# Optimization experiments

Measured on AMD Instinct MI355X. Metric: run time of the kernel, lower is better.

The kernel has to match this reference:

```python
import jax, jax.numpy as jnp
import numpy as np

NUM_CLASSES = 80
CONF_THRE = 0.2
NMS_THRE = 0.45
MAX_DET = 300   # fixed cap replacing torch's variable-length NMS output (padded + keep mask)
IMG = 640.0


def setup_inputs() -> dict:
    key = jax.random.key(0)
    k1, k2 = jax.random.split(key)
    pred = jax.random.uniform(k1, (32, 8400, 85), dtype=jnp.float32)
    # scale cx,cy,w,h to pixel range so IoU/NMS geometry is realistic
    pred = pred.at[..., :4].multiply(IMG)
    zone = jax.random.uniform(k2, (8, 2), dtype=jnp.float32) * IMG
    return {"prediction": pred, "zone": zone}


def _pairwise_iou(b):
    # b: [B, K, 4] in x1y1x2y2
    area = jnp.clip(b[..., 2] - b[..., 0], 0.0) * jnp.clip(b[..., 3] - b[..., 1], 0.0)
    lt = jnp.maximum(b[:, :, None, :2], b[:, None, :, :2])
    rb = jnp.minimum(b[:, :, None, 2:], b[:, None, :, 2:])
    wh = jnp.clip(rb - lt, 0.0)
    inter = wh[..., 0] * wh[..., 1]
    return inter / (area[:, :, None] + area[:, None, :] - inter + 1e-9)


def _postprocess(prediction):
    # decode cx,cy,w,h -> x1,y1,x2,y2
    xy = prediction[..., :2]
    wh = prediction[..., 2:4]
    boxes = jnp.concatenate([xy - wh * 0.5, xy + wh * 0.5], axis=-1)  # [B,N,4]
    obj = prediction[..., 4]                                           # [B,N]
    cls = prediction[..., 5:5 + NUM_CLASSES]
    class_conf = jnp.max(cls, axis=-1)                                 # [B,N]
    class_pred = jnp.argmax(cls, axis=-1)                              # [B,N]

    # confidence mask (obj * class_conf >= thre); invalid -> -inf so top_k drops them
    nms_score = obj * class_conf
    nms_score = jnp.where(nms_score >= CONF_THRE, nms_score, -jnp.inf)

    s, idx = jax.lax.top_k(nms_score, MAX_DET)                         # [B,K]
    b = jnp.take_along_axis(boxes, idx[..., None], axis=1)             # [B,K,4]

    # class-agnostic greedy NMS on score-sorted boxes (matches torchvision.ops.nms)
    iou = _pairwise_iou(b)                                             # [B,K,K]
    keep = jnp.isfinite(s)                                             # valid (passed conf) entries
    ar = jnp.arange(MAX_DET)
    def body(i, keep):
        sup = keep[:, i][:, None] & (iou[:, i, :] > NMS_THRE) & (ar > i)
        return keep & jnp.logical_not(sup)
    keep = jax.lax.fori_loop(0, MAX_DET, body, keep)

    obj_s = jnp.take_along_axis(obj, idx, axis=1)
    conf_s = jnp.take_along_axis(class_conf, idx, axis=1)
    cls_s = jnp.take_along_axis(class_pred, idx, axis=1).astype(jnp.int32)
    # extract_boxes_scores_and_classes: score = max over columns [obj, class_conf]
    scores = jnp.maximum(obj_s, conf_s)
    return b, scores, cls_s, keep


def _points_inside_zone(px, py, zone):
    # px, py: [B,K]; zone: [Z,2]. Ray-casting parity test (faithful to torch version).
    zr = jnp.roll(zone, shift=1, axis=0)
    xi, yi = zone[:, 0], zone[:, 1]
    xj, yj = zr[:, 0], zr[:, 1]
    pyb = py[..., None]  # [B,K,1] vs [Z]
    pxb = px[..., None]
    gyi = yi > pyb
    gyj = yj > pyb
    gx = (xj - xi) * (pyb - yi) / (yj - yi) + xi
    inter = (gyi != gyj) & (gx > pxb)
    return (jnp.sum(inter.astype(jnp.int32), axis=-1) % 2) > 0


def reference(prediction, zone):
    b, scores, classes, keep = _postprocess(prediction)
    cx = (b[..., 0] + b[..., 2]) * 0.5
    cy = (b[..., 1] + b[..., 3]) * 0.5
    in_zone = _points_inside_zone(cx, cy, zone) & keep
    centers_yx = jnp.stack([cy, cx], axis=-1)                          # [B,K,2]
    boxes_yxyx = jnp.stack([b[..., 1], b[..., 0], b[..., 3], b[..., 2]], axis=-1)
    return boxes_yxyx, in_zone, scores, classes, centers_yx, keep
```

## Files before the change

### kernel.cpp

```cpp
#include <hip/hip_runtime.h>
#include <stdint.h>

typedef unsigned long long ull;

#define NA 8400
#define NB 32
#define KTOP 300
#define NC 80
#define CH 33

#define O1 38400
#define O2 48000
#define O3 57600
#define O4 67200
#define O5 86400

__global__ __launch_bounds__(256) void score_kernel(const float* __restrict__ pred,
                                                    uint32_t* __restrict__ keys) {
    __shared__ float sP[128 * 85];
    const int blk = blockIdx.x;
    const float4* g4 = (const float4*)(pred + (size_t)blk * 128 * 85);
    float4* l4 = (float4*)sP;
    for (int i = threadIdx.x; i < (128 * 85 / 4); i += 256) l4[i] = g4[i];
    __syncthreads();
    const int t = threadIdx.x;
    if (t < 128) {
        const float* p = sP + t * 85;
        float obj = p[4];
        float b0 = p[5], b1 = p[6], b2 = p[7], b3 = p[8];
        #pragma unroll
        for (int c = 4; c < NC; c += 4) {
            b0 = fmaxf(b0, p[5 + c]);
            b1 = fmaxf(b1, p[6 + c]);
            b2 = fmaxf(b2, p[7 + c]);
            b3 = fmaxf(b3, p[8 + c]);
        }
        float best = fmaxf(fmaxf(b0, b1), fmaxf(b2, b3));
        float sc = obj * best;
        uint32_t u = (sc >= 0.2f) ? (__float_as_uint(sc) | 0x80000000u) : 0x007FFFFFu;
        keys[(size_t)blk * 128 + t] = u;
    }
}

__global__ __launch_bounds__(256) void batch_kernel(const float* __restrict__ pred,
                                                    const float* __restrict__ zone,
                                                    const uint32_t* __restrict__ keys,
                                                    float* __restrict__ out) {
    #pragma clang fp contract(off)
    __shared__ union {
        uint32_t keys[8448];
        struct {
            float b0[KTOP], b1[KTOP], b2[KTOP], b3[KTOP];
            ull mask[KTOP * 5];
        } late;
    } u;
    __shared__ ull sSel[KTOP];
    __shared__ ull sSorted[KTOP];
    __shared__ uint32_t sH[8 * 257];
    __shared__ uint32_t sTot[4];
    __shared__ uint32_t sBc[2];
    __shared__ int sCnt;
    __shared__ ull sKeepF[5];
    __shared__ float sZone[16];

    const int b = blockIdx.x;
    const int t = threadIdx.x;
    const int lane = t & 63;
    const int wv = t >> 6;
    const int hc = t >> 5;

    {
        const uint4* g4 = (const uint4*)(keys + (size_t)b * NA);
        uint4* l4 = (uint4*)u.keys;
        for (int i = t; i < NA / 4; i += 256) l4[i] = g4[i];
        for (int e = NA + t; e < 8448; e += 256) u.keys[e] = 0u;
    }
    if (t < 16) sZone[t] = zone[t];
    if (t == 0) sCnt = 0;
    __syncthreads();

    uint32_t prefix = 0, r = KTOP;
    const int beg = t * CH;
    const int end = (beg + CH < NA) ? beg + CH : NA;
    for (int round = 0; round < 4; ++round) {
        const int shift = 24 - 8 * round;
        for (int i = t; i < 8 * 257; i += 256) sH[i] = 0u;
        __syncthreads();
        const uint32_t pmask = (round == 0) ? 0u : (0xFFFFFFFFu << (shift + 8));
        for (int e = beg; e < end; ++e) {
            uint32_t k = u.keys[e];
            if ((k & pmask) == (prefix & pmask))
                atomicAdd(&sH[hc * 257 + ((k >> shift) & 0xFFu)], 1u);
        }
        __syncthreads();
        uint32_t v = 0;
        #pragma unroll
        for (int c = 0; c < 8; ++c) v += sH[c * 257 + t];
        uint32_t s = v;
        #pragma unroll
        for (int off = 1; off < 64; off <<= 1) {
            uint32_t o = __shfl_down(s, off, 64);
            if (lane + off < 64) s += o;
        }
        if (lane == 0) sTot[wv] = s;
        __syncthreads();
        uint32_t S = s;
        #pragma unroll
        for (int w2 = 0; w2 < 4; ++w2) if (w2 > wv) S += sTot[w2];
        uint32_t above = S - v;
        if (above < r && S >= r) {
            sBc[0] = prefix | ((uint32_t)t << shift);
            sBc[1] = r - above;
        }
        __syncthreads();
        prefix = sBc[0]; r = sBc[1];
    }
    const uint32_t kth = prefix;
    const uint32_t rem = r;
    const uint32_t cntgt = KTOP - rem;

    {
        uint32_t eqc = 0;
        for (int e = beg; e < end; ++e) {
            uint32_t k = u.keys[e];
            if (k > kth) {
                int p = atomicAdd(&sCnt, 1);
                sSel[p] = ((ull)k << 32) | (ull)(0xFFFFFFFFu - (uint32_t)e);
            } else if (k == kth) eqc++;
        }
        uint32_t ps = eqc;
        #pragma unroll
        for (int off = 1; off < 64; off <<= 1) {
            uint32_t o = __shfl_up(ps, off, 64);
            if (lane >= off) ps += o;
        }
        if (lane == 63) sTot[wv] = ps;
        __syncthreads();
        uint32_t off0 = ps - eqc;
        #pragma unroll
        for (int w2 = 0; w2 < 4; ++w2) if (w2 < wv) off0 += sTot[w2];
        for (int e = beg; e < end; ++e) {
            uint32_t k = u.keys[e];
            if (k == kth) {
                if (off0 < rem)
                    sSel[cntgt + off0] = ((ull)k << 32) | (ull)(0xFFFFFFFFu - (uint32_t)e);
                off0++;
            }
        }
        __syncthreads();
    }

    {
        ull my0 = sSel[t];
        ull my1 = (t < KTOP - 256) ? sSel[256 + t] : 0ull;
        int r0 = 0, r1 = 0;
        for (int j = 0; j < KTOP; ++j) {
            ull v = sSel[j];
            r0 += (v > my0) ? 1 : 0;
            r1 += (v > my1) ? 1 : 0;
        }
        sSorted[r0] = my0;
        if (t < KTOP - 256) sSorted[r1] = my1;
        __syncthreads();
    }

    for (int i = t; i < KTOP; i += 256) {
        uint32_t a = 0xFFFFFFFFu - (uint32_t)sSorted[i];
        const float* p = pred + ((size_t)b * NA + a) * 85;
        float x = p[0], y = p[1], w = p[2], h = p[3];
        float hw = w * 0.5f, hh = h * 0.5f;
        u.late.b0[i] = x - hw; u.late.b1[i] = y - hh;
        u.late.b2[i] = x + hw; u.late.b3[i] = y + hh;
    }
    __syncthreads();

    for (int role = 0; role < 5; ++role) {
        const int j0 = role * 64;
        int jmax = j0 + 64; if (jmax > KTOP) jmax = KTOP;
        for (int i = t; i < KTOP; i += 256) {
            float x1 = u.late.b0[i], y1 = u.late.b1[i], x2 = u.late.b2[i], y2 = u.late.b3[i];
            float ai = fmaxf(x2 - x1, 0.0f) * fmaxf(y2 - y1, 0.0f);
            ull bits = 0ull;
            int jbeg = (j0 > i + 1) ? j0 : (i + 1);
            for (int j = jbeg; j < jmax; ++j) {
                float bx1 = u.late.b0[j], by1 = u.late.b1[j], bx2 = u.late.b2[j], by2 = u.late.b3[j];
                float aj = fmaxf(bx2 - bx1, 0.0f) * fmaxf(by2 - by1, 0.0f);
                float iw = fminf(x2, bx2) - fmaxf(x1, bx1); iw = fmaxf(iw, 0.0f);
                float ih = fminf(y2, by2) - fmaxf(y1, by1); ih = fmaxf(ih, 0.0f);
                float inter = iw * ih;
                float den = ai + aj;
                den = den - inter;
                den = den + 1e-9f;
                float iou = inter / den;
                if (iou > 0.45f) bits |= (1ull << (j - j0));
            }
            u.late.mask[i * 5 + role] = bits;
        }
    }
    __syncthreads();

    if (wv == 0) {
        ull rm[5][5];
        ull kw[5];
        #pragma unroll
        for (int w = 0; w < 5; ++w) {
            int i = w * 64 + lane;
            bool f = (i < KTOP) && (((uint32_t)(sSorted[i] >> 32)) > 0x007FFFFFu);
            kw[w] = __ballot(f);
            #pragma unroll
            for (int ww = 0; ww < 5; ++ww)
                rm[w][ww] = (i < KTOP) ? u.late.mask[i * 5 + ww] : 0ull;
        }
        #pragma unroll
        for (int w = 0; w < 5; ++w) {
            ull cur = kw[w];
            while (cur) {
                int ib = __builtin_ctzll(cur);
                ull m0 = __shfl(rm[w][0], ib);
                ull m1 = __shfl(rm[w][1], ib);
                ull m2 = __shfl(rm[w][2], ib);
                ull m3 = __shfl(rm[w][3], ib);
                ull m4 = __shfl(rm[w][4], ib);
                kw[0] &= ~m0; kw[1] &= ~m1; kw[2] &= ~m2; kw[3] &= ~m3; kw[4] &= ~m4;
                ull done = (ib == 63) ? 0ull : (~0ull << (ib + 1));
                cur = kw[w] & done;
            }
        }
        if (lane == 0) {
            #pragma unroll
            for (int w = 0; w < 5; ++w) sKeepF[w] = kw[w];
        }
    } else {
        const size_t bo = (size_t)b * KTOP;
        for (int i = t - 64; i < KTOP; i += 192) {
            uint32_t a = 0xFFFFFFFFu - (uint32_t)sSorted[i];
            const float* p = pred + ((size_t)b * NA + a) * 85;
            float x = p[0], y = p[1], w = p[2], h = p[3], obj = p[4];
            float best = p[5]; int bc = 0;
            for (int c = 1; c < NC; ++c) {
                float v = p[5 + c];
                if (v > best) { best = v; bc = c; }
            }
            float hw = w * 0.5f, hh = h * 0.5f;
            float x1 = x - hw, y1 = y - hh, x2 = x + hw, y2 = y + hh;
            out[(bo + i) * 4 + 0] = y1;
            out[(bo + i) * 4 + 1] = x1;
            out[(bo + i) * 4 + 2] = y2;
            out[(bo + i) * 4 + 3] = x2;
            out[O4 + (bo + i) * 2 + 0] = (y1 + y2) * 0.5f;
            out[O4 + (bo + i) * 2 + 1] = (x1 + x2) * 0.5f;
            out[O2 + bo + i] = fmaxf(obj, best);
            out[O3 + bo + i] = (float)bc;
        }
    }
    __syncthreads();

    const size_t bo = (size_t)b * KTOP;
    for (int i = t; i < KTOP; i += 256) {
        int kp = (int)((sKeepF[i >> 6] >> (i & 63)) & 1ull);
        float cy = (u.late.b1[i] + u.late.b3[i]) * 0.5f;
        float cx = (u.late.b0[i] + u.late.b2[i]) * 0.5f;
        int cnt = 0;
        #pragma unroll
        for (int e = 0; e < 8; ++e) {
            float xi = sZone[2 * e], yi = sZone[2 * e + 1];
            int ep = (e + 7) & 7;
            float xj = sZone[2 * ep], yj = sZone[2 * ep + 1];
            bool gyi = yi > cy, gyj = yj > cy;
            if (gyi != gyj) {
                float gx = (xj - xi) * (cy - yi) / (yj - yi) + xi;
                if (gx > cx) cnt++;
            }
        }
        int inz = (((cnt & 1) != 0) && kp) ? 1 : 0;
        out[O1 + bo + i] = (float)inz;
        out[O5 + bo + i] = (float)kp;
    }
}

extern "C" void kernel_launch(void* const* d_in, const int* in_sizes, int n_in,
                              void* d_out, int out_size, void* d_ws, size_t ws_size,
                              hipStream_t stream) {
    const float* pred = (const float*)d_in[0];
    const float* zone = (const float*)d_in[1];
    float* out = (float*)d_out;
    uint32_t* keys = (uint32_t*)d_ws;

    score_kernel<<<(NB * NA) / 128, 256, 0, stream>>>(pred, keys);
    batch_kernel<<<NB, 256, 0, stream>>>(pred, zone, keys, out);
}
```

Baseline: 226.6 us.

## Widen per-batch kernel to 1024 threads and parallelize selection and IoU stages

The per-image kernel now runs 1024 threads per block instead of 256. That shortens each thread's radix-select scan chunk from 33 to 9 elements and uses 16 histogram copies to spread atomic contention. The IoU mask stage is flattened over (row, role) pairs, and output writing plus class argmax move before the NMS stage so every thread does its share. Since only 32 blocks run, this adds parallelism inside each block to fill a sparsely used GPU, at the cost of more barrier overhead and higher register pressure.

Result: faster. 200.3 us (-11.6%).

```diff
diff --git a/kernel.cpp b/kernel.cpp
--- a/kernel.cpp
+++ b/kernel.cpp
@@ -7,7 +7,9 @@
 #define NB 32
 #define KTOP 300
 #define NC 80
-#define CH 33
+#define CH 9
+#define NCOPY 16
+#define HSTRIDE 257
 
 #define O1 38400
 #define O2 48000
@@ -42,10 +44,10 @@
     }
 }
 
-__global__ __launch_bounds__(256) void batch_kernel(const float* __restrict__ pred,
-                                                    const float* __restrict__ zone,
-                                                    const uint32_t* __restrict__ keys,
-                                                    float* __restrict__ out) {
+__global__ __launch_bounds__(1024) void batch_kernel(const float* __restrict__ pred,
+                                                     const float* __restrict__ zone,
+                                                     const uint32_t* __restrict__ keys,
+                                                     float* __restrict__ out) {
     #pragma clang fp contract(off)
     __shared__ union {
         uint32_t keys[8448];
@@ -56,8 +58,9 @@
     } u;
     __shared__ ull sSel[KTOP];
     __shared__ ull sSorted[KTOP];
-    __shared__ uint32_t sH[8 * 257];
-    __shared__ uint32_t sTot[4];
+    __shared__ uint32_t sH[NCOPY * HSTRIDE];
+    __shared__ uint32_t sWTot[16];
+    __shared__ uint32_t sTot4[4];
     __shared__ uint32_t sBc[2];
     __shared__ int sCnt;
     __shared__ ull sKeepF[5];
@@ -67,13 +70,11 @@
     const int t = threadIdx.x;
     const int lane = t & 63;
     const int wv = t >> 6;
-    const int hc = t >> 5;
 
     {
         const uint4* g4 = (const uint4*)(keys + (size_t)b * NA);
         uint4* l4 = (uint4*)u.keys;
-        for (int i = t; i < NA / 4; i += 256) l4[i] = g4[i];
-        for (int e = NA + t; e < 8448; e += 256) u.keys[e] = 0u;
+        for (int i = t; i < NA / 4; i += 1024) l4[i] = g4[i];
     }
     if (t < 16) sZone[t] = zone[t];
     if (t == 0) sCnt = 0;
@@ -84,33 +85,38 @@
     const int end = (beg + CH < NA) ? beg + CH : NA;
     for (int round = 0; round < 4; ++round) {
         const int shift = 24 - 8 * round;
-        for (int i = t; i < 8 * 257; i += 256) sH[i] = 0u;
+        for (int i = t; i < NCOPY * HSTRIDE; i += 1024) sH[i] = 0u;
         __syncthreads();
         const uint32_t pmask = (round == 0) ? 0u : (0xFFFFFFFFu << (shift + 8));
         for (int e = beg; e < end; ++e) {
             uint32_t k = u.keys[e];
             if ((k & pmask) == (prefix & pmask))
-                atomicAdd(&sH[hc * 257 + ((k >> shift) & 0xFFu)], 1u);
-        }
-        __syncthreads();
-        uint32_t v = 0;
-        #pragma unroll
-        for (int c = 0; c < 8; ++c) v += sH[c * 257 + t];
-        uint32_t s = v;
-        #pragma unroll
-        for (int off = 1; off < 64; off <<= 1) {
-            uint32_t o = __shfl_down(s, off, 64);
-            if (lane + off < 64) s += o;
-        }
-        if (lane == 0) sTot[wv] = s;
-        __syncthreads();
-        uint32_t S = s;
-        #pragma unroll
-        for (int w2 = 0; w2 < 4; ++w2) if (w2 > wv) S += sTot[w2];
-        uint32_t above = S - v;
-        if (above < r && S >= r) {
-            sBc[0] = prefix | ((uint32_t)t << shift);
-            sBc[1] = r - above;
+                atomicAdd(&sH[wv * HSTRIDE + ((k >> shift) & 0xFFu)], 1u);
+        }
+        __syncthreads();
+        uint32_t v = 0, s = 0;
+        if (t < 256) {
+            #pragma unroll
+            for (int c = 0; c < NCOPY; ++c) v += sH[c * HSTRIDE + t];
+            s = v;
+            #pragma unroll
+            for (int off = 1; off < 64; off <<= 1) {
+                uint32_t o = __shfl_down(s, off, 64);
+                if (lane + off < 64) s += o;
+            }
+            if (lane == 0) sTot4[t >> 6] = s;
+        }
+        __syncthreads();
+        if (t < 256) {
+            uint32_t S = s;
+            const int w4 = t >> 6;
+            #pragma unroll
+            for (int w2 = 0; w2 < 4; ++w2) if (w2 > w4) S += sTot4[w2];
+            uint32_t above = S - v;
+            if (above < r && S >= r) {
+                sBc[0] = prefix | ((uint32_t)t << shift);
+                sBc[1] = r - above;
+            }
         }
         __syncthreads();
         prefix = sBc[0]; r = sBc[1];
@@ -134,11 +140,11 @@
             uint32_t o = __shfl_up(ps, off, 64);
             if (lane >= off) ps += o;
         }
-        if (lane == 63) sTot[wv] = ps;
+        if (lane == 63) sWTot[wv] = ps;
         __syncthreads();
         uint32_t off0 = ps - eqc;
         #pragma unroll
-        for (int w2 = 0; w2 < 4; ++w2) if (w2 < wv) off0 += sTot[w2];
+        for (int w2 = 0; w2 < 16; ++w2) if (w2 < wv) off0 += sWTot[w2];
         for (int e = beg; e < end; ++e) {
             uint32_t k = u.keys[e];
             if (k == kth) {
@@ -150,52 +156,64 @@
         __syncthreads();
     }
 
-    {
-        ull my0 = sSel[t];
-        ull my1 = (t < KTOP - 256) ? sSel[256 + t] : 0ull;
-        int r0 = 0, r1 = 0;
+    if (t < KTOP) {
+        ull my = sSel[t];
+        int rk = 0;
         for (int j = 0; j < KTOP; ++j) {
             ull v = sSel[j];
-            r0 += (v > my0) ? 1 : 0;
-            r1 += (v > my1) ? 1 : 0;
-        }
-        sSorted[r0] = my0;
-        if (t < KTOP - 256) sSorted[r1] = my1;
-        __syncthreads();
-    }
-
-    for (int i = t; i < KTOP; i += 256) {
-        uint32_t a = 0xFFFFFFFFu - (uint32_t)sSorted[i];
+            rk += (v > my) ? 1 : 0;
+        }
+        sSorted[rk] = my;
+    }
+    __syncthreads();
+
+    const size_t bo = (size_t)b * KTOP;
+    if (t < KTOP) {
+        uint32_t a = 0xFFFFFFFFu - (uint32_t)sSorted[t];
         const float* p = pred + ((size_t)b * NA + a) * 85;
-        float x = p[0], y = p[1], w = p[2], h = p[3];
+        float x = p[0], y = p[1], w = p[2], h = p[3], obj = p[4];
+        float best = p[5]; int bc = 0;
+        for (int c = 1; c < NC; ++c) {
+            float v = p[5 + c];
+            if (v > best) { best = v; bc = c; }
+        }
         float hw = w * 0.5f, hh = h * 0.5f;
-        u.late.b0[i] = x - hw; u.late.b1[i] = y - hh;
-        u.late.b2[i] = x + hw; u.late.b3[i] = y + hh;
-    }
-    __syncthreads();
-
-    for (int role = 0; role < 5; ++role) {
+        float x1 = x - hw, y1 = y - hh, x2 = x + hw, y2 = y + hh;
+        u.late.b0[t] = x1; u.late.b1[t] = y1;
+        u.late.b2[t] = x2; u.late.b3[t] = y2;
+        out[(bo + t) * 4 + 0] = y1;
+        out[(bo + t) * 4 + 1] = x1;
+        out[(bo + t) * 4 + 2] = y2;
+        out[(bo + t) * 4 + 3] = x2;
+        out[O4 + (bo + t) * 2 + 0] = (y1 + y2) * 0.5f;
+        out[O4 + (bo + t) * 2 + 1] = (x1 + x2) * 0.5f;
+        out[O2 + bo + t] = fmaxf(obj, best);
+        out[O3 + bo + t] = (float)bc;
+    }
+    __syncthreads();
+
+    for (int p = t; p < KTOP * 5; p += 1024) {
+        const int i = p / 5;
+        const int role = p % 5;
         const int j0 = role * 64;
         int jmax = j0 + 64; if (jmax > KTOP) jmax = KTOP;
-        for (int i = t; i < KTOP; i += 256) {
-            float x1 = u.late.b0[i], y1 = u.late.b1[i], x2 = u.late.b2[i], y2 = u.late.b3[i];
-            float ai = fmaxf(x2 - x1, 0.0f) * fmaxf(y2 - y1, 0.0f);
-            ull bits = 0ull;
-            int jbeg = (j0 > i + 1) ? j0 : (i + 1);
-            for (int j = jbeg; j < jmax; ++j) {
-                float bx1 = u.late.b0[j], by1 = u.late.b1[j], bx2 = u.late.b2[j], by2 = u.late.b3[j];
-                float aj = fmaxf(bx2 - bx1, 0.0f) * fmaxf(by2 - by1, 0.0f);
-                float iw = fminf(x2, bx2) - fmaxf(x1, bx1); iw = fmaxf(iw, 0.0f);
-                float ih = fminf(y2, by2) - fmaxf(y1, by1); ih = fmaxf(ih, 0.0f);
-                float inter = iw * ih;
-                float den = ai + aj;
-                den = den - inter;
-                den = den + 1e-9f;
-                float iou = inter / den;
-                if (iou > 0.45f) bits |= (1ull << (j - j0));
-            }
-            u.late.mask[i * 5 + role] = bits;
-        }
+        float x1 = u.late.b0[i], y1 = u.late.b1[i], x2 = u.late.b2[i], y2 = u.late.b3[i];
+        float ai = fmaxf(x2 - x1, 0.0f) * fmaxf(y2 - y1, 0.0f);
+        ull bits = 0ull;
+        int jbeg = (j0 > i + 1) ? j0 : (i + 1);
+        for (int j = jbeg; j < jmax; ++j) {
+            float bx1 = u.late.b0[j], by1 = u.late.b1[j], bx2 = u.late.b2[j], by2 = u.late.b3[j];
+            float aj = fmaxf(bx2 - bx1, 0.0f) * fmaxf(by2 - by1, 0.0f);
+            float iw = fminf(x2, bx2) - fmaxf(x1, bx1); iw = fmaxf(iw, 0.0f);
+            float ih = fminf(y2, by2) - fmaxf(y1, by1); ih = fmaxf(ih, 0.0f);
+            float inter = iw * ih;
+            float den = ai + aj;
+            den = den - inter;
+            den = den + 1e-9f;
+            float iou = inter / den;
+            if (iou > 0.45f) bits |= (1ull << (j - j0));
+        }
+        u.late.mask[p] = bits;
     }
     __syncthreads();
 
@@ -230,36 +248,13 @@
             #pragma unroll
             for (int w = 0; w < 5; ++w) sKeepF[w] = kw[w];
         }
-    } else {
-        const size_t bo = (size_t)b * KTOP;
-        for (int i = t - 64; i < KTOP; i += 192) {
-            uint32_t a = 0xFFFFFFFFu - (uint32_t)sSorted[i];
-            const float* p = pred + ((size_t)b * NA + a) * 85;
-            float x = p[0], y = p[1], w = p[2], h = p[3], obj = p[4];
-            float best = p[5]; int bc = 0;
-            for (int c = 1; c < NC; ++c) {
-                float v = p[5 + c];
-                if (v > best) { best = v; bc = c; }
-            }
-            float hw = w * 0.5f, hh = h * 0.5f;
-            float x1 = x - hw, y1 = y - hh, x2 = x + hw, y2 = y + hh;
-            out[(bo + i) * 4 + 0] = y1;
-            out[(bo + i) * 4 + 1] = x1;
-            out[(bo + i) * 4 + 2] = y2;
-            out[(bo + i) * 4 + 3] = x2;
-            out[O4 + (bo + i) * 2 + 0] = (y1 + y2) * 0.5f;
-            out[O4 + (bo + i) * 2 + 1] = (x1 + x2) * 0.5f;
-            out[O2 + bo + i] = fmaxf(obj, best);
-            out[O3 + bo + i] = (float)bc;
-        }
-    }
-    __syncthreads();
-
-    const size_t bo = (size_t)b * KTOP;
-    for (int i = t; i < KTOP; i += 256) {
-        int kp = (int)((sKeepF[i >> 6] >> (i & 63)) & 1ull);
-        float cy = (u.late.b1[i] + u.late.b3[i]) * 0.5f;
-        float cx = (u.late.b0[i] + u.late.b2[i]) * 0.5f;
+    }
+    __syncthreads();
+
+    if (t < KTOP) {
+        int kp = (int)((sKeepF[t >> 6] >> (t & 63)) & 1ull);
+        float cy = (u.late.b1[t] + u.late.b3[t]) * 0.5f;
+        float cx = (u.late.b0[t] + u.late.b2[t]) * 0.5f;
         int cnt = 0;
         #pragma unroll
         for (int e = 0; e < 8; ++e) {
@@ -273,8 +268,8 @@
             }
         }
         int inz = (((cnt & 1) != 0) && kp) ? 1 : 0;
-        out[O1 + bo + i] = (float)inz;
-        out[O5 + bo + i] = (float)kp;
+        out[O1 + bo + t] = (float)inz;
+        out[O5 + bo + t] = (float)kp;
     }
 }
 
@@ -287,5 +282,5 @@
     uint32_t* keys = (uint32_t*)d_ws;
 
     score_kernel<<<(NB * NA) / 128, 256, 0, stream>>>(pred, keys);
-    batch_kernel<<<NB, 256, 0, stream>>>(pred, zone, keys, out);
+    batch_kernel<<<NB, 1024, 0, stream>>>(pred, zone, keys, out);
 }
```
